# Kernel optimization log

Hardware: AMD Instinct MI355X
Metric: run time of the kernel (lower is better)

## Reference

```python
import jax, jax.numpy as jnp
import numpy as np

NUM_HEADS = 16

def setup_inputs() -> dict:
    key = jax.random.key(0)
    ks = jax.random.split(key, 6)
    B, S, D = 4, 2048, 1024
    sc = 1.0 / np.sqrt(D)
    return {
        "x": jax.random.normal(ks[0], (B, S, D), jnp.float32),
        "Wq": jax.random.normal(ks[1], (D, D), jnp.float32) * sc,
        "Wk": jax.random.normal(ks[2], (D, D), jnp.float32) * sc,
        "Wv": jax.random.normal(ks[3], (D, D), jnp.float32) * sc,
        "Wo": jax.random.normal(ks[4], (D, D), jnp.float32) * sc,
        "bo": jnp.zeros((D,), jnp.float32),
    }

def reference(x, Wq, Wk, Wv, Wo, bo):
    B, S, D = x.shape
    H = NUM_HEADS
    hd = D // H
    # projections (Linear: x @ W^T, but we store W as [d_in, d_out] so x @ W)
    q = (x @ Wq).reshape(B, S, H, hd)
    k = (x @ Wk).reshape(B, S, H, hd)
    v = (x @ Wv).reshape(B, S, H, hd)
    # scores: [B, H, S, S]
    scores = jnp.einsum("bqhd,bkhd->bhqk", q, k) / jnp.sqrt(jnp.asarray(hd, x.dtype))
    attn = jax.nn.softmax(scores, axis=-1)  # dropout p=0.0 (eval) -> identity
    ctx = jnp.einsum("bhqk,bkhd->bqhd", attn, v).reshape(B, S, D)
    return ctx @ Wo + bo
```

## Files before the change

### kernel.cpp

```cpp
#include <hip/hip_runtime.h>
#include <hip/hip_bf16.h>

typedef __bf16 bf16x8 __attribute__((ext_vector_type(8)));
typedef float f32x4 __attribute__((ext_vector_type(4)));

#define D_MODEL 1024
#define SEQ 2048
#define BATCH 4
#define HEADS 16
#define HD 64
#define M_TOT (BATCH * SEQ)
#define QPW 4

static __device__ __forceinline__ unsigned short f2bf(float f) {
  unsigned int u = __float_as_uint(f);
  unsigned int lsb = (u >> 16) & 1u;
  u += 0x7fffu + lsb;
  return (unsigned short)(u >> 16);
}

__global__ __launch_bounds__(256) void cvt_x_kernel(const float* __restrict__ x,
                                                    unsigned short* __restrict__ xb,
                                                    int n4) {
  int i = blockIdx.x * 256 + threadIdx.x;
  if (i >= n4) return;
  const float4 v = reinterpret_cast<const float4*>(x)[i];
  ushort4 o;
  o.x = f2bf(v.x); o.y = f2bf(v.y); o.z = f2bf(v.z); o.w = f2bf(v.w);
  reinterpret_cast<ushort4*>(xb)[i] = o;
}

__global__ __launch_bounds__(256) void transW_kernel(const float* __restrict__ W,
                                                     unsigned short* __restrict__ Wt) {
  __shared__ float t[32][33];
  int bx = blockIdx.x * 32;
  int by = blockIdx.y * 32;
  int tx = threadIdx.x, ty = threadIdx.y;
#pragma unroll
  for (int i = 0; i < 32; i += 8)
    t[ty + i][tx] = W[(size_t)(by + ty + i) * D_MODEL + bx + tx];
  __syncthreads();
#pragma unroll
  for (int i = 0; i < 32; i += 8)
    Wt[(size_t)(bx + ty + i) * D_MODEL + by + tx] = f2bf(t[tx][ty + i]);
}

template <int MODE>
__global__ __launch_bounds__(256) void gemm_bt_kernel(
    const unsigned short* __restrict__ A, const unsigned short* __restrict__ Bt,
    void* __restrict__ out, const float* __restrict__ bias, int M, int N, int K,
    float scale) {
  __shared__ __align__(16) unsigned short Als[128][72];
  __shared__ __align__(16) unsigned short Bls[128][72];

  const int tid = threadIdx.x;
  const int l = tid & 63;
  const int wave = tid >> 6;
  const int l15 = l & 15;
  const int lk = l >> 4;
  const int wm = wave >> 1, wn = wave & 1;

  const int nblocks_n = N >> 7;
  const int mblk = blockIdx.x / nblocks_n;
  const int nblk = blockIdx.x % nblocks_n;
  const int m0 = mblk << 7, n0 = nblk << 7;

  f32x4 acc[4][4] = {};

  const int srow = tid >> 3;
  const int scol = (tid & 7) * 8;

  bf16x8 areg[4], breg[4];
#pragma unroll
  for (int i = 0; i < 4; ++i) {
    areg[i] = *reinterpret_cast<const bf16x8*>(&A[(size_t)(m0 + srow + i * 32) * K + scol]);
    breg[i] = *reinterpret_cast<const bf16x8*>(&Bt[(size_t)(n0 + srow + i * 32) * K + scol]);
  }

  for (int k0 = 0; k0 < K; k0 += 64) {
    __syncthreads();
#pragma unroll
    for (int i = 0; i < 4; ++i) {
      *reinterpret_cast<bf16x8*>(&Als[srow + i * 32][scol]) = areg[i];
      *reinterpret_cast<bf16x8*>(&Bls[srow + i * 32][scol]) = breg[i];
    }
    __syncthreads();

    if (k0 + 64 < K) {
#pragma unroll
      for (int i = 0; i < 4; ++i) {
        areg[i] = *reinterpret_cast<const bf16x8*>(
            &A[(size_t)(m0 + srow + i * 32) * K + k0 + 64 + scol]);
        breg[i] = *reinterpret_cast<const bf16x8*>(
            &Bt[(size_t)(n0 + srow + i * 32) * K + k0 + 64 + scol]);
      }
    }

#pragma unroll
    for (int kk = 0; kk < 2; ++kk) {
      bf16x8 af[4], bfr[4];
#pragma unroll
      for (int m = 0; m < 4; ++m)
        af[m] = *reinterpret_cast<const bf16x8*>(&Als[wm * 64 + m * 16 + l15][kk * 32 + lk * 8]);
#pragma unroll
      for (int n = 0; n < 4; ++n)
        bfr[n] = *reinterpret_cast<const bf16x8*>(&Bls[wn * 64 + n * 16 + l15][kk * 32 + lk * 8]);
#pragma unroll
      for (int m = 0; m < 4; ++m)
#pragma unroll
        for (int n = 0; n < 4; ++n)
          acc[m][n] = __builtin_amdgcn_mfma_f32_16x16x32_bf16(af[m], bfr[n], acc[m][n], 0, 0, 0);
    }
  }

#pragma unroll
  for (int m = 0; m < 4; ++m) {
#pragma unroll
    for (int n = 0; n < 4; ++n) {
      const int row0 = wm * 64 + m * 16 + lk * 4;
      const int col = wn * 64 + n * 16 + l15;
      const int gm0 = m0 + row0;
      const int gn = n0 + col;
      if (MODE == 0) {
        unsigned short* o = (unsigned short*)out;
#pragma unroll
        for (int r = 0; r < 4; ++r)
          o[(size_t)(gm0 + r) * N + gn] = f2bf(acc[m][n][r] * scale);
      } else if (MODE == 1) {
        unsigned short* o = (unsigned short*)out;
        int b = gm0 >> 11, s = gm0 & 2047;
        int h = gn >> 6, d = gn & 63;
        size_t base = ((size_t)((b * HEADS + h) * HD + d)) * SEQ + s;
#pragma unroll
        for (int r = 0; r < 4; ++r) o[base + r] = f2bf(acc[m][n][r]);
      } else {
        float* o = (float*)out;
        float bv = bias[gn];
#pragma unroll
        for (int r = 0; r < 4; ++r)
          o[(size_t)(gm0 + r) * N + gn] = acc[m][n][r] + bv;
      }
    }
  }
}

__global__ __launch_bounds__(256) void attn_kernel(const unsigned short* __restrict__ Q,
                                                   const unsigned short* __restrict__ Kb,
                                                   const unsigned short* __restrict__ Vt,
                                                   unsigned short* __restrict__ ctx) {
  __shared__ __align__(16) unsigned short Kls[2][64 * 64];
  __shared__ __align__(16) unsigned short Vls[2][64 * 64];

  const int tid = threadIdx.x;
  const int l = tid & 63;
  const int wave = tid >> 6;
  const int l15 = l & 15;
  const int lk = l >> 4;

  const int bid = blockIdx.x;
  const int nid = (bid & 7) * 64 + (bid >> 3);
  const int qt = nid & 7;
  const int bh = nid >> 3;
  const int b = bh >> 4;
  const int h = bh & 15;

  const int qbase = b * SEQ + qt * 256 + wave * 64;

  bf16x8 qf[QPW][2];
#pragma unroll
  for (int qb = 0; qb < QPW; ++qb)
#pragma unroll
    for (int kk = 0; kk < 2; ++kk)
      qf[qb][kk] = *reinterpret_cast<const bf16x8*>(
          &Q[(size_t)(qbase + qb * 16 + l15) * D_MODEL + h * HD + kk * 32 + lk * 8]);

  f32x4 acc[QPW][4] = {};
  float lsum[QPW] = {};

  const int srow = tid >> 2;
  const int sc = tid & 3;
  const int krow = (srow & 32) | ((srow & 4) << 2) | ((srow >> 1) & 12) | (srow & 3);

  const size_t kgbase = ((size_t)b * SEQ) * D_MODEL + h * HD;
  const size_t vgbase = ((size_t)(b * HEADS + h) * HD) * SEQ;

  uint4 kreg[2], vreg[2];
#pragma unroll
  for (int i = 0; i < 2; ++i) {
    kreg[i] = *reinterpret_cast<const uint4*>(
        &Kb[kgbase + (size_t)srow * D_MODEL + sc * 8 + i * 32]);
    vreg[i] = *reinterpret_cast<const uint4*>(
        &Vt[vgbase + (size_t)srow * SEQ + sc * 8 + i * 32]);
  }

  int p = 0;
  for (int kt = 0; kt < SEQ / 64; ++kt) {
    char* klsb = (char*)Kls[p];
    char* vlsb = (char*)Vls[p];
#pragma unroll
    for (int i = 0; i < 2; ++i) {
      *reinterpret_cast<uint4*>(
          klsb + krow * 128 + ((sc * 16 + i * 64) ^ ((krow & 7) << 4))) = kreg[i];
      *reinterpret_cast<uint4*>(
          vlsb + srow * 128 + ((sc * 16 + i * 64) ^ ((srow & 7) << 4))) = vreg[i];
    }
    __syncthreads();

    if (kt + 1 < SEQ / 64) {
      const int nt = kt + 1;
#pragma unroll
      for (int i = 0; i < 2; ++i) {
        kreg[i] = *reinterpret_cast<const uint4*>(
            &Kb[kgbase + (size_t)(nt * 64 + srow) * D_MODEL + sc * 8 + i * 32]);
        vreg[i] = *reinterpret_cast<const uint4*>(
            &Vt[vgbase + (size_t)srow * SEQ + nt * 64 + sc * 8 + i * 32]);
      }
    }

    f32x4 s[QPW][4] = {};
#pragma unroll
    for (int kk = 0; kk < 2; ++kk) {
      bf16x8 kf[4];
#pragma unroll
      for (int n = 0; n < 4; ++n)
        kf[n] = *reinterpret_cast<const bf16x8*>(
            klsb + (n * 16 + l15) * 128 + ((kk * 64 + lk * 16) ^ ((l15 & 7) << 4)));
#pragma unroll
      for (int qb = 0; qb < QPW; ++qb)
#pragma unroll
        for (int n = 0; n < 4; ++n)
          s[qb][n] = __builtin_amdgcn_mfma_f32_16x16x32_bf16(kf[n], qf[qb][kk], s[qb][n], 0, 0, 0);
    }

    bf16x8 pvv[QPW][2];
#pragma unroll
    for (int qb = 0; qb < QPW; ++qb) {
      float ps = 0.f;
#pragma unroll
      for (int n = 0; n < 4; ++n)
#pragma unroll
        for (int r = 0; r < 4; ++r) {
          float pp = __builtin_amdgcn_exp2f(s[qb][n][r]);
          ps += pp;
          pvv[qb][n >> 1][(n & 1) * 4 + r] = (__bf16)pp;
        }
      lsum[qb] += ps;
    }

#pragma unroll
    for (int kk = 0; kk < 2; ++kk) {
      bf16x8 vf[4];
#pragma unroll
      for (int nd = 0; nd < 4; ++nd)
        vf[nd] = *reinterpret_cast<const bf16x8*>(
            vlsb + (nd * 16 + l15) * 128 + ((kk * 64 + lk * 16) ^ ((l15 & 7) << 4)));
#pragma unroll
      for (int qb = 0; qb < QPW; ++qb)
#pragma unroll
        for (int nd = 0; nd < 4; ++nd)
          acc[qb][nd] = __builtin_amdgcn_mfma_f32_16x16x32_bf16(vf[nd], pvv[qb][kk], acc[qb][nd], 0, 0, 0);
    }
    p ^= 1;
  }

#pragma unroll
  for (int qb = 0; qb < QPW; ++qb) {
    float t = lsum[qb];
    t += __shfl_xor(t, 16);
    t += __shfl_xor(t, 32);
    const float inv = 1.0f / t;
    const size_t row = (size_t)(qbase + qb * 16 + l15) * D_MODEL + h * HD;
#pragma unroll
    for (int nd = 0; nd < 4; ++nd) {
      ushort4 ov;
      ov.x = f2bf(acc[qb][nd][0] * inv);
      ov.y = f2bf(acc[qb][nd][1] * inv);
      ov.z = f2bf(acc[qb][nd][2] * inv);
      ov.w = f2bf(acc[qb][nd][3] * inv);
      *reinterpret_cast<ushort4*>(&ctx[row + nd * 16 + lk * 4]) = ov;
    }
  }
}

extern "C" void kernel_launch(void* const* d_in, const int* in_sizes, int n_in,
                              void* d_out, int out_size, void* d_ws, size_t ws_size,
                              hipStream_t stream) {
  const float* x = (const float*)d_in[0];
  const float* Wq = (const float*)d_in[1];
  const float* Wk = (const float*)d_in[2];
  const float* Wv = (const float*)d_in[3];
  const float* Wo = (const float*)d_in[4];
  const float* bo = (const float*)d_in[5];

  char* ws = (char*)d_ws;
  const size_t MB = 1u << 20;
  unsigned short* xb = (unsigned short*)(ws + 0 * MB);
  unsigned short* WqT = (unsigned short*)(ws + 16 * MB);
  unsigned short* WkT = (unsigned short*)(ws + 18 * MB);
  unsigned short* WvT = (unsigned short*)(ws + 20 * MB);
  unsigned short* WoT = (unsigned short*)(ws + 22 * MB);
  unsigned short* Qb = (unsigned short*)(ws + 24 * MB);
  unsigned short* Kb = (unsigned short*)(ws + 40 * MB);
  unsigned short* Vt = (unsigned short*)(ws + 56 * MB);
  unsigned short* ctx = (unsigned short*)(ws + 72 * MB);

  int n4 = (M_TOT * D_MODEL) / 4;
  cvt_x_kernel<<<n4 / 256, 256, 0, stream>>>(x, xb, n4);

  dim3 tb(32, 8);
  dim3 tg(32, 32);
  transW_kernel<<<tg, tb, 0, stream>>>(Wq, WqT);
  transW_kernel<<<tg, tb, 0, stream>>>(Wk, WkT);
  transW_kernel<<<tg, tb, 0, stream>>>(Wv, WvT);
  transW_kernel<<<tg, tb, 0, stream>>>(Wo, WoT);

  int gblocks = (M_TOT / 128) * (D_MODEL / 128);
  gemm_bt_kernel<0><<<gblocks, 256, 0, stream>>>(xb, WqT, Qb, nullptr, M_TOT, D_MODEL, D_MODEL,
                                                 0.125f * 1.44269504f);
  gemm_bt_kernel<0><<<gblocks, 256, 0, stream>>>(xb, WkT, Kb, nullptr, M_TOT, D_MODEL, D_MODEL, 1.0f);
  gemm_bt_kernel<1><<<gblocks, 256, 0, stream>>>(xb, WvT, Vt, nullptr, M_TOT, D_MODEL, D_MODEL, 1.0f);

  attn_kernel<<<BATCH * HEADS * (SEQ / 256), 256, 0, stream>>>(Qb, Kb, Vt, ctx);

  gemm_bt_kernel<2><<<gblocks, 256, 0, stream>>>(ctx, WoT, d_out, bo, M_TOT, D_MODEL, D_MODEL, 1.0f);
}
```

Measured before the change: 233.0 us.

## Split attention over two key halves and merge partial results in a combine kernel

The attention grid is doubled: each block now handles half of the key/value sequence for its query tile. Each half writes its own normalized bf16 output and its row sums, reusing buffers that are no longer needed (xb for the second half's output, the WqT region for the sums). A new combine kernel blends the two halves by weighting them with their row sums. This raises the number of blocks to fill the GPU better, at the cost of an extra launch, more global memory traffic and a second bf16 rounding of the output.

```diff
diff --git a/kernel.cpp b/kernel.cpp
--- a/kernel.cpp
+++ b/kernel.cpp
@@ -147,7 +147,10 @@
 __global__ __launch_bounds__(256) void attn_kernel(const unsigned short* __restrict__ Q,
                                                    const unsigned short* __restrict__ Kb,
                                                    const unsigned short* __restrict__ Vt,
-                                                   unsigned short* __restrict__ ctx) {
+                                                   unsigned short* __restrict__ o0,
+                                                   unsigned short* __restrict__ o1,
+                                                   float* __restrict__ l0,
+                                                   float* __restrict__ l1) {
   __shared__ __align__(16) unsigned short Kls[2][64 * 64];
   __shared__ __align__(16) unsigned short Vls[2][64 * 64];
 
@@ -158,13 +161,15 @@
   const int lk = l >> 4;
 
   const int bid = blockIdx.x;
-  const int nid = (bid & 7) * 64 + (bid >> 3);
-  const int qt = nid & 7;
-  const int bh = nid >> 3;
+  const int nid = (bid & 7) * 128 + (bid >> 3);
+  const int ks = nid & 1;
+  const int qt = (nid >> 1) & 7;
+  const int bh = nid >> 4;
   const int b = bh >> 4;
   const int h = bh & 15;
 
   const int qbase = b * SEQ + qt * 256 + wave * 64;
+  const int kt0 = ks * 16;
 
   bf16x8 qf[QPW][2];
 #pragma unroll
@@ -188,13 +193,13 @@
 #pragma unroll
   for (int i = 0; i < 2; ++i) {
     kreg[i] = *reinterpret_cast<const uint4*>(
-        &Kb[kgbase + (size_t)srow * D_MODEL + sc * 8 + i * 32]);
+        &Kb[kgbase + (size_t)(kt0 * 64 + srow) * D_MODEL + sc * 8 + i * 32]);
     vreg[i] = *reinterpret_cast<const uint4*>(
-        &Vt[vgbase + (size_t)srow * SEQ + sc * 8 + i * 32]);
+        &Vt[vgbase + (size_t)srow * SEQ + kt0 * 64 + sc * 8 + i * 32]);
   }
 
   int p = 0;
-  for (int kt = 0; kt < SEQ / 64; ++kt) {
+  for (int kt = kt0; kt < kt0 + 16; ++kt) {
     char* klsb = (char*)Kls[p];
     char* vlsb = (char*)Vls[p];
 #pragma unroll
@@ -206,7 +211,7 @@
     }
     __syncthreads();
 
-    if (kt + 1 < SEQ / 64) {
+    if (kt + 1 < kt0 + 16) {
       const int nt = kt + 1;
 #pragma unroll
       for (int i = 0; i < 2; ++i) {
@@ -263,13 +268,16 @@
     p ^= 1;
   }
 
+  unsigned short* op = ks ? o1 : o0;
+  float* lp = ks ? l1 : l0;
 #pragma unroll
   for (int qb = 0; qb < QPW; ++qb) {
     float t = lsum[qb];
     t += __shfl_xor(t, 16);
     t += __shfl_xor(t, 32);
     const float inv = 1.0f / t;
-    const size_t row = (size_t)(qbase + qb * 16 + l15) * D_MODEL + h * HD;
+    const int grow = qbase + qb * 16 + l15;
+    const size_t row = (size_t)grow * D_MODEL + h * HD;
 #pragma unroll
     for (int nd = 0; nd < 4; ++nd) {
       ushort4 ov;
@@ -277,9 +285,42 @@
       ov.y = f2bf(acc[qb][nd][1] * inv);
       ov.z = f2bf(acc[qb][nd][2] * inv);
       ov.w = f2bf(acc[qb][nd][3] * inv);
-      *reinterpret_cast<ushort4*>(&ctx[row + nd * 16 + lk * 4]) = ov;
-    }
-  }
+      *reinterpret_cast<ushort4*>(&op[row + nd * 16 + lk * 4]) = ov;
+    }
+    if (l < 16) lp[grow * HEADS + h] = t;
+  }
+}
+
+static __device__ __forceinline__ unsigned int comb2(unsigned int u0, unsigned int u1,
+                                                     float w0, float w1) {
+  float a0 = __uint_as_float((u0 & 0xffffu) << 16);
+  float b0 = __uint_as_float(u0 & 0xffff0000u);
+  float a1 = __uint_as_float((u1 & 0xffffu) << 16);
+  float b1 = __uint_as_float(u1 & 0xffff0000u);
+  unsigned int lo = f2bf(a0 * w0 + a1 * w1);
+  unsigned int hi = f2bf(b0 * w0 + b1 * w1);
+  return lo | (hi << 16);
+}
+
+__global__ __launch_bounds__(256) void combine_kernel(unsigned short* __restrict__ o0,
+                                                      const unsigned short* __restrict__ o1,
+                                                      const float* __restrict__ l0,
+                                                      const float* __restrict__ l1) {
+  const int i = blockIdx.x * 256 + threadIdx.x;
+  const int row = i >> 7;
+  const int h = (i & 127) >> 3;
+  const float a = l0[row * HEADS + h];
+  const float b = l1[row * HEADS + h];
+  const float inv = 1.0f / (a + b);
+  const float w0 = a * inv, w1 = b * inv;
+  const uint4 x0 = reinterpret_cast<const uint4*>(o0)[i];
+  const uint4 x1 = reinterpret_cast<const uint4*>(o1)[i];
+  uint4 y;
+  y.x = comb2(x0.x, x1.x, w0, w1);
+  y.y = comb2(x0.y, x1.y, w0, w1);
+  y.z = comb2(x0.z, x1.z, w0, w1);
+  y.w = comb2(x0.w, x1.w, w0, w1);
+  reinterpret_cast<uint4*>(o0)[i] = y;
 }
 
 extern "C" void kernel_launch(void* const* d_in, const int* in_sizes, int n_in,
@@ -303,6 +344,8 @@
   unsigned short* Kb = (unsigned short*)(ws + 40 * MB);
   unsigned short* Vt = (unsigned short*)(ws + 56 * MB);
   unsigned short* ctx = (unsigned short*)(ws + 72 * MB);
+  float* l0 = (float*)(ws + 16 * MB);
+  float* l1 = (float*)(ws + 16 * MB + 512 * 1024);
 
   int n4 = (M_TOT * D_MODEL) / 4;
   cvt_x_kernel<<<n4 / 256, 256, 0, stream>>>(x, xb, n4);
@@ -320,7 +363,8 @@
   gemm_bt_kernel<0><<<gblocks, 256, 0, stream>>>(xb, WkT, Kb, nullptr, M_TOT, D_MODEL, D_MODEL, 1.0f);
   gemm_bt_kernel<1><<<gblocks, 256, 0, stream>>>(xb, WvT, Vt, nullptr, M_TOT, D_MODEL, D_MODEL, 1.0f);
 
-  attn_kernel<<<BATCH * HEADS * (SEQ / 256), 256, 0, stream>>>(Qb, Kb, Vt, ctx);
+  attn_kernel<<<BATCH * HEADS * (SEQ / 256) * 2, 256, 0, stream>>>(Qb, Kb, Vt, ctx, xb, l0, l1);
+  combine_kernel<<<(M_TOT * D_MODEL / 8) / 256, 256, 0, stream>>>(ctx, xb, l0, l1);
 
   gemm_bt_kernel<2><<<gblocks, 256, 0, stream>>>(ctx, WoT, d_out, bo, M_TOT, D_MODEL, D_MODEL, 1.0f);
 }
```

After: 270.1 us. 1.16x slower.
